# Optimization experiments

Hardware: AMD Instinct MI355X
Metric: run time of the kernel (lower is better)

## Reference

```python
import jax, jax.numpy as jnp
import numpy as np

N_NODES = 50000
N_EDGES = 400000
D_IN = 128
D_H = 128
N_CLASSES = 20
N_GRAPHS = 256
EPS_BN = 1e-5


def _lin_params(key, d_in, d_out, scale=0.05):
    kw, kb = jax.random.split(key)
    W = jax.random.normal(kw, (d_in, d_out), jnp.float32) * scale
    b = jax.random.normal(kb, (d_out,), jnp.float32) * scale
    return W, b


def setup_inputs() -> dict:
    key = jax.random.key(0)
    ks = jax.random.split(key, 20)
    inp = {
        "x": jax.random.normal(ks[0], (N_NODES, D_IN), jnp.float32),
        "edge_index": jax.random.randint(ks[1], (2, N_EDGES), 0, N_NODES, jnp.int32),
        "batch": jnp.sort(jax.random.randint(ks[2], (N_NODES,), 0, N_GRAPHS, jnp.int32)),
    }
    kidx = 3
    for li, d_in in zip((1, 2, 3), (D_IN, D_H, D_H)):
        for nm in ("q", "k", "v", "s"):
            W, b = _lin_params(ks[kidx], d_in, D_H)
            kidx += 1
            inp[f"W{nm}{li}"] = W
            inp[f"b{nm}{li}"] = b
        inp[f"gamma{li}"] = jnp.ones((D_H,), jnp.float32)
        inp[f"beta{li}"] = jnp.zeros((D_H,), jnp.float32)
    Wl, bl = _lin_params(ks[kidx], D_H, N_CLASSES)
    inp["Wlin"] = Wl
    inp["blin"] = bl
    return inp


def _segment_softmax(logits, seg, n):
    m = jax.ops.segment_max(logits, seg, num_segments=n)
    e = jnp.exp(logits - m[seg])
    s = jax.ops.segment_sum(e, seg, num_segments=n)
    return e / (s[seg] + 1e-16)


def _transformer_conv(x, src, dst, Wq, bq, Wk, bk, Wv, bv, Ws, bs):
    # heads=1, concat=True, root_weight=True (PyG TransformerConv defaults)
    q = x @ Wq + bq  # [N, d]
    k = x @ Wk + bk
    v = x @ Wv + bv
    d = q.shape[-1]
    logits = jnp.sum(q[dst] * k[src], axis=-1) / jnp.sqrt(jnp.float32(d))  # [E]
    alpha = _segment_softmax(logits, dst, x.shape[0])
    out = jax.ops.segment_sum(alpha[:, None] * v[src], dst, num_segments=x.shape[0])
    return out + x @ Ws + bs


def _batch_norm(x, gamma, beta):
    mu = jnp.mean(x, axis=0)
    var = jnp.var(x, axis=0)
    return gamma * (x - mu) * jax.lax.rsqrt(var + EPS_BN) + beta


def _global_mean_pool(x, batch, n_graphs):
    sums = jax.ops.segment_sum(x, batch, num_segments=n_graphs)
    cnt = jax.ops.segment_sum(jnp.ones((x.shape[0],), x.dtype), batch, num_segments=n_graphs)
    return sums / jnp.maximum(cnt, 1.0)[:, None]


def reference(x, edge_index, batch,
              Wq1, bq1, Wk1, bk1, Wv1, bv1, Ws1, bs1, gamma1, beta1,
              Wq2, bq2, Wk2, bk2, Wv2, bv2, Ws2, bs2, gamma2, beta2,
              Wq3, bq3, Wk3, bk3, Wv3, bv3, Ws3, bs3, gamma3, beta3,
              Wlin, blin):
    src, dst = edge_index[0], edge_index[1]
    h = _transformer_conv(x, src, dst, Wq1, bq1, Wk1, bk1, Wv1, bv1, Ws1, bs1)
    h = jax.nn.relu(_batch_norm(h, gamma1, beta1))  # dropout inactive (eval)
    h = _transformer_conv(h, src, dst, Wq2, bq2, Wk2, bk2, Wv2, bv2, Ws2, bs2)
    h = jax.nn.relu(_batch_norm(h, gamma2, beta2))
    h = _transformer_conv(h, src, dst, Wq3, bq3, Wk3, bk3, Wv3, bv3, Ws3, bs3)
    h = jax.nn.relu(_batch_norm(h, gamma3, beta3))
    g = _global_mean_pool(h, batch, N_GRAPHS)  # [G, d]
    return g @ Wlin + blin  # [G, num_classes]
```

## Files before the change

### kernel.cpp

```cpp
#include <hip/hip_runtime.h>

#define N_NODES 50000
#define N_EDGES 400000
#define DH 128
#define N_GRAPHS 256

#define SCAN_CHUNK 512
#define N_CHUNKS ((N_NODES + SCAN_CHUNK - 1) / SCAN_CHUNK)
#define ATTN_BLOCKS ((N_NODES + 15) / 16)
#define POOL_CHUNKS ((N_NODES + 63) / 64)

typedef __bf16 bf16x8 __attribute__((ext_vector_type(8)));
typedef float f32x4 __attribute__((ext_vector_type(4)));
typedef _Float16 f16x2 __attribute__((ext_vector_type(2)));
typedef _Float16 f16x8 __attribute__((ext_vector_type(8)));

#define DEV __device__ __forceinline__

#if defined(__has_builtin)
#if __has_builtin(__builtin_amdgcn_fdot2)
#define HAS_FDOT2 1
#endif
#endif

DEV float fdot2acc(f16x2 a, f16x2 b, float c) {
#ifdef HAS_FDOT2
  return __builtin_amdgcn_fdot2(a, b, c, false);
#else
  return (float)a.x * (float)b.x + (float)a.y * (float)b.y + c;
#endif
}

DEV unsigned short f2bf(float f) {
  union { float f; unsigned int i; } v; v.f = f;
  unsigned int x = v.i;
  unsigned int r = (x + 0x7fffu + ((x >> 16) & 1u)) >> 16;
  return (unsigned short)r;
}

struct WPtrs { const float* w[12]; };

__global__ void repack_kernel(WPtrs wp, unsigned short* __restrict__ WB,
                              int* __restrict__ deg, int* __restrict__ counter, int N) {
  int mat = blockIdx.y;
  int m = blockIdx.x * 256 + threadIdx.x;
  int j = m & 7;
  int lane = (m >> 3) & 63;
  int ct = (m >> 9) & 7;
  int kk = m >> 12;
  int i = kk * 32 + (lane >> 4) * 8 + j;
  int o = ct * 16 + (lane & 15);
  WB[mat * 16384 + m] = f2bf(wp.w[mat][i * 128 + o]);
  if (mat == 0) {
    for (int idx = m; idx < N; idx += 16384) deg[idx] = 0;
    if (m == 0) *counter = 0;
  }
}

__global__ void deg_count(const int* __restrict__ ei, int* __restrict__ deg, int E) {
  int e = blockIdx.x * 256 + threadIdx.x;
  if (e < E) atomicAdd(&deg[ei[E + e]], 1);
}

__global__ __launch_bounds__(256) void scan_sum(const int* __restrict__ deg,
                                                int* __restrict__ partials, int N) {
  __shared__ int red[256];
  int b = blockIdx.x, t = threadIdx.x;
  int base = b * SCAN_CHUNK + t * 2;
  int s = 0;
  if (base + 1 < N) { int2 v = *reinterpret_cast<const int2*>(deg + base); s = v.x + v.y; }
  else if (base < N) s = deg[base];
  red[t] = s;
  __syncthreads();
  for (int off = 128; off; off >>= 1) {
    if (t < off) red[t] += red[t + off];
    __syncthreads();
  }
  if (t == 0) partials[b] = red[0];
}

__global__ __launch_bounds__(128) void scan_partials(int* __restrict__ partials) {
  __shared__ int s[128];
  int t = threadIdx.x;
  int v = (t < N_CHUNKS) ? partials[t] : 0;
  s[t] = v;
  __syncthreads();
  for (int off = 1; off < 128; off <<= 1) {
    int o = (t >= off) ? s[t - off] : 0;
    __syncthreads();
    s[t] += o;
    __syncthreads();
  }
  if (t < N_CHUNKS) partials[t] = s[t] - v;
}

__global__ __launch_bounds__(256) void scan_apply(const int* __restrict__ deg,
                                                  const int* __restrict__ partials,
                                                  int* __restrict__ rowptr,
                                                  int* __restrict__ cursor, int N, int E) {
  __shared__ int s[256];
  int b = blockIdx.x, t = threadIdx.x;
  int base = b * SCAN_CHUNK + t * 2;
  int d0 = 0, d1 = 0;
  if (base + 1 < N) { int2 v = *reinterpret_cast<const int2*>(deg + base); d0 = v.x; d1 = v.y; }
  else if (base < N) d0 = deg[base];
  int local = d0 + d1;
  s[t] = local;
  __syncthreads();
  for (int off = 1; off < 256; off <<= 1) {
    int o = (t >= off) ? s[t - off] : 0;
    __syncthreads();
    s[t] += o;
    __syncthreads();
  }
  int offp = partials[b] + s[t] - local;
  if (base < N)     { rowptr[base] = offp;          cursor[base] = offp; }
  if (base + 1 < N) { rowptr[base + 1] = offp + d0; cursor[base + 1] = offp + d0; }
  if (b == 0 && t == 0) rowptr[N] = E;
}

__global__ void csr_scatter(const int* __restrict__ ei, int* __restrict__ cursor,
                            int* __restrict__ adj, int E) {
  int e = blockIdx.x * 256 + threadIdx.x;
  if (e < E) {
    int dst = ei[E + e];
    int pos = atomicAdd(&cursor[dst], 1);
    adj[pos] = ei[e];
  }
}

struct GemmOut { _Float16* Y[4]; const float* bias[4]; };

#define LDP 136

__global__ __launch_bounds__(256) void gemm_proj(
    const float* __restrict__ Xf,
    const _Float16* __restrict__ Hin,
    const float* __restrict__ scale, const float* __restrict__ shift,
    const unsigned short* __restrict__ WB4,
    GemmOut go, int useBN, int N)
{
  __shared__ __align__(16) unsigned short xs[64 * LDP];

  const int t = threadIdx.x;
  const int rowBase = blockIdx.x * 64;
  const int igc = (t & 15) * 8;

  if (useBN) {
    float4 sc0 = *reinterpret_cast<const float4*>(scale + igc);
    float4 sc1 = *reinterpret_cast<const float4*>(scale + igc + 4);
    float4 sh0 = *reinterpret_cast<const float4*>(shift + igc);
    float4 sh1 = *reinterpret_cast<const float4*>(shift + igc + 4);
#pragma unroll
    for (int j = 0; j < 4; ++j) {
      int v = t + 256 * j;
      int r = v >> 4;
      int grow = rowBase + r;
      ushort4 o0 = make_ushort4(0, 0, 0, 0), o1 = make_ushort4(0, 0, 0, 0);
      if (grow < N) {
        f16x8 hv = *reinterpret_cast<const f16x8*>(Hin + (size_t)grow * 128 + igc);
        o0.x = f2bf(fmaxf((float)hv[0] * sc0.x + sh0.x, 0.f));
        o0.y = f2bf(fmaxf((float)hv[1] * sc0.y + sh0.y, 0.f));
        o0.z = f2bf(fmaxf((float)hv[2] * sc0.z + sh0.z, 0.f));
        o0.w = f2bf(fmaxf((float)hv[3] * sc0.w + sh0.w, 0.f));
        o1.x = f2bf(fmaxf((float)hv[4] * sc1.x + sh1.x, 0.f));
        o1.y = f2bf(fmaxf((float)hv[5] * sc1.y + sh1.y, 0.f));
        o1.z = f2bf(fmaxf((float)hv[6] * sc1.z + sh1.z, 0.f));
        o1.w = f2bf(fmaxf((float)hv[7] * sc1.w + sh1.w, 0.f));
      }
      *reinterpret_cast<ushort4*>(&xs[r * LDP + igc]) = o0;
      *reinterpret_cast<ushort4*>(&xs[r * LDP + igc + 4]) = o1;
    }
  } else {
#pragma unroll
    for (int j = 0; j < 4; ++j) {
      int v = t + 256 * j;
      int r = v >> 4;
      int grow = rowBase + r;
      ushort4 o0 = make_ushort4(0, 0, 0, 0), o1 = make_ushort4(0, 0, 0, 0);
      if (grow < N) {
        float4 a = *reinterpret_cast<const float4*>(Xf + (size_t)grow * 128 + igc);
        float4 b = *reinterpret_cast<const float4*>(Xf + (size_t)grow * 128 + igc + 4);
        o0.x = f2bf(a.x); o0.y = f2bf(a.y); o0.z = f2bf(a.z); o0.w = f2bf(a.w);
        o1.x = f2bf(b.x); o1.y = f2bf(b.y); o1.z = f2bf(b.z); o1.w = f2bf(b.w);
      }
      *reinterpret_cast<ushort4*>(&xs[r * LDP + igc]) = o0;
      *reinterpret_cast<ushort4*>(&xs[r * LDP + igc + 4]) = o1;
    }
  }
  __syncthreads();

  const int wave = t >> 6;
  const int lane = t & 63;
  const int ln16 = lane & 15;
  const int quad = lane >> 4;
  const int r0 = wave * 16;

  bf16x8 afrag[4];
#pragma unroll
  for (int kk = 0; kk < 4; ++kk)
    afrag[kk] = *reinterpret_cast<const bf16x8*>(&xs[(r0 + ln16) * LDP + kk * 32 + quad * 8]);

  for (int proj = 0; proj < 4; ++proj) {
    const unsigned short* __restrict__ WB = WB4 + proj * 16384;
    const float* __restrict__ bias = go.bias[proj];

    f32x4 acc[8] = {};
#pragma unroll
    for (int kk = 0; kk < 4; ++kk) {
#pragma unroll
      for (int ct = 0; ct < 8; ++ct) {
        bf16x8 b = *reinterpret_cast<const bf16x8*>(WB + ((kk * 8 + ct) * 64 + lane) * 8);
        acc[ct] = __builtin_amdgcn_mfma_f32_16x16x32_bf16(afrag[kk], b, acc[ct], 0, 0, 0);
      }
    }

    _Float16* __restrict__ Yh = go.Y[proj];
#pragma unroll
    for (int ct = 0; ct < 8; ++ct) {
      int col = ct * 16 + ln16;
      float bv = bias[col];
#pragma unroll
      for (int reg = 0; reg < 4; ++reg) {
        int grow = rowBase + r0 + quad * 4 + reg;
        if (grow < N) Yh[(size_t)grow * 128 + col] = (_Float16)(acc[ct][reg] + bv);
      }
    }
  }
}

__global__ __launch_bounds__(256) void node_attn(
    const int* __restrict__ rowptr, const int* __restrict__ adj,
    const _Float16* __restrict__ Q, const _Float16* __restrict__ K,
    const _Float16* __restrict__ V, _Float16* __restrict__ H,
    float* __restrict__ Pbuf, int N)
{
  __shared__ float lsum[16][128];
  __shared__ float lsq[16][128];
  int t = threadIdx.x;
  int w = t >> 4, lane = t & 15;
  int n = blockIdx.x * 16 + w;
  bool valid = n < N;
  int nn = valid ? n : 0;
  int p0 = 0, p1 = 0;
  if (valid) { p0 = rowptr[n]; p1 = rowptr[n + 1]; }

  f16x8 qv = *reinterpret_cast<const f16x8*>(Q + (size_t)nn * 128 + lane * 8);
  f16x2 q0 = {qv[0], qv[1]}, q1 = {qv[2], qv[3]}, q2 = {qv[4], qv[5]}, q3 = {qv[6], qv[7]};

  float m = -INFINITY, s = 0.f;
  float acc[8] = {};

  int p = p0;
  for (; p + 1 < p1; p += 2) {
    int s0 = adj[p], s1 = adj[p + 1];
    f16x8 k0 = *reinterpret_cast<const f16x8*>(K + (size_t)s0 * 128 + lane * 8);
    f16x8 k1 = *reinterpret_cast<const f16x8*>(K + (size_t)s1 * 128 + lane * 8);
    float d0 = fdot2acc(q0, (f16x2){k0[0], k0[1]},
               fdot2acc(q1, (f16x2){k0[2], k0[3]},
               fdot2acc(q2, (f16x2){k0[4], k0[5]},
               fdot2acc(q3, (f16x2){k0[6], k0[7]}, 0.f))));
    float d1 = fdot2acc(q0, (f16x2){k1[0], k1[1]},
               fdot2acc(q1, (f16x2){k1[2], k1[3]},
               fdot2acc(q2, (f16x2){k1[4], k1[5]},
               fdot2acc(q3, (f16x2){k1[6], k1[7]}, 0.f))));
#pragma unroll
    for (int off = 8; off; off >>= 1) {
      d0 += __shfl_xor(d0, off, 16);
      d1 += __shfl_xor(d1, off, 16);
    }
    float l0 = d0 * 0.08838834764831845f;
    float l1 = d1 * 0.08838834764831845f;
    float mn = fmaxf(m, fmaxf(l0, l1));
    float sc = __expf(m - mn);
    float w0 = __expf(l0 - mn);
    float w1 = __expf(l1 - mn);
    f16x8 v0 = *reinterpret_cast<const f16x8*>(V + (size_t)s0 * 128 + lane * 8);
    f16x8 v1 = *reinterpret_cast<const f16x8*>(V + (size_t)s1 * 128 + lane * 8);
#pragma unroll
    for (int i = 0; i < 8; ++i)
      acc[i] = acc[i] * sc + w0 * (float)v0[i] + w1 * (float)v1[i];
    s = s * sc + w0 + w1;
    m = mn;
  }
  if (p < p1) {
    int s0 = adj[p];
    f16x8 k0 = *reinterpret_cast<const f16x8*>(K + (size_t)s0 * 128 + lane * 8);
    float d0 = fdot2acc(q0, (f16x2){k0[0], k0[1]},
               fdot2acc(q1, (f16x2){k0[2], k0[3]},
               fdot2acc(q2, (f16x2){k0[4], k0[5]},
               fdot2acc(q3, (f16x2){k0[6], k0[7]}, 0.f))));
#pragma unroll
    for (int off = 8; off; off >>= 1) d0 += __shfl_xor(d0, off, 16);
    float l0 = d0 * 0.08838834764831845f;
    float mn = fmaxf(m, l0);
    float sc = __expf(m - mn);
    float w0 = __expf(l0 - mn);
    f16x8 v0 = *reinterpret_cast<const f16x8*>(V + (size_t)s0 * 128 + lane * 8);
#pragma unroll
    for (int i = 0; i < 8; ++i)
      acc[i] = acc[i] * sc + w0 * (float)v0[i];
    s = s * sc + w0;
    m = mn;
  }

  float h[8];
#pragma unroll
  for (int i = 0; i < 8; ++i) h[i] = 0.f;
  if (valid) {
    float inv = 1.0f / (s + 1e-16f);
    f16x8 hh = *reinterpret_cast<const f16x8*>(H + (size_t)n * 128 + lane * 8);
    f16x8 ho;
#pragma unroll
    for (int i = 0; i < 8; ++i) {
      h[i] = (float)hh[i] + acc[i] * inv;
      ho[i] = (_Float16)h[i];
    }
    *reinterpret_cast<f16x8*>(H + (size_t)n * 128 + lane * 8) = ho;
  }

#pragma unroll
  for (int i = 0; i < 8; i += 4) {
    float4 hv = make_float4(h[i], h[i + 1], h[i + 2], h[i + 3]);
    float4 h2 = make_float4(hv.x * hv.x, hv.y * hv.y, hv.z * hv.z, hv.w * hv.w);
    *reinterpret_cast<float4*>(&lsum[w][lane * 8 + i]) = hv;
    *reinterpret_cast<float4*>(&lsq[w][lane * 8 + i]) = h2;
  }
  __syncthreads();

  int f = t & 127;
  float a = 0.f;
  if (t < 128) {
#pragma unroll
    for (int n16 = 0; n16 < 16; ++n16) a += lsum[n16][f];
  } else {
#pragma unroll
    for (int n16 = 0; n16 < 16; ++n16) a += lsq[n16][f];
  }
  Pbuf[(size_t)blockIdx.x * 256 + t] = a;
}

__global__ __launch_bounds__(256) void bn_reduce(
    const float* __restrict__ Pbuf, float* __restrict__ partial,
    int* __restrict__ counter,
    const float* __restrict__ gamma, const float* __restrict__ beta,
    float* __restrict__ scale, float* __restrict__ shift, int N)
{
  int t = threadIdx.x;
  float s0 = 0.f, s1 = 0.f, s2 = 0.f, s3 = 0.f;
  int r = blockIdx.x;
  for (; r + 192 < ATTN_BLOCKS; r += 256) {
    s0 += Pbuf[(size_t)(r      ) * 256 + t];
    s1 += Pbuf[(size_t)(r +  64) * 256 + t];
    s2 += Pbuf[(size_t)(r + 128) * 256 + t];
    s3 += Pbuf[(size_t)(r + 192) * 256 + t];
  }
  for (; r < ATTN_BLOCKS; r += 64) s0 += Pbuf[(size_t)r * 256 + t];
  partial[blockIdx.x * 256 + t] = s0 + s1 + s2 + s3;

  __threadfence();
  __shared__ int isLast;
  if (t == 0) isLast = (atomicAdd(counter, 1) == 63);
  __syncthreads();
  if (!isLast) return;
  __threadfence();

  __shared__ float red[256];
  float a0 = 0.f, a1 = 0.f, a2 = 0.f, a3 = 0.f;
#pragma unroll
  for (int b = 0; b < 64; b += 4) {
    a0 += partial[(b + 0) * 256 + t];
    a1 += partial[(b + 1) * 256 + t];
    a2 += partial[(b + 2) * 256 + t];
    a3 += partial[(b + 3) * 256 + t];
  }
  red[t] = a0 + a1 + a2 + a3;
  __syncthreads();
  if (t == 0) *counter = 0;
  if (t < 128) {
    float mean = red[t] / (float)N;
    float var = red[t + 128] / (float)N - mean * mean;
    var = fmaxf(var, 0.f);
    float sc = gamma[t] * rsqrtf(var + 1e-5f);
    scale[t] = sc;
    shift[t] = beta[t] - mean * sc;
  }
}

__global__ __launch_bounds__(256) void pool_chunk(
    const _Float16* __restrict__ H, const float* __restrict__ scale,
    const float* __restrict__ shift, const int* __restrict__ batch,
    float* __restrict__ pooled, int N)
{
  int f = threadIdx.x & 127, half = threadIdx.x >> 7;
  int base = blockIdx.x * 64;
  int lim = min(base + 64, N);
  float sc = scale[f], sh = shift[f];
  int curg = -1; float s = 0.f;
  for (int row = base + half; row < lim; row += 2) {
    int g = batch[row];
    if (g != curg) {
      if (curg >= 0) unsafeAtomicAdd(pooled + curg * 128 + f, s);
      curg = g; s = 0.f;
    }
    s += fmaxf((float)H[(size_t)row * 128 + f] * sc + sh, 0.f);
  }
  if (curg >= 0) unsafeAtomicAdd(pooled + curg * 128 + f, s);
}

__global__ __launch_bounds__(64) void final_linear(
    const float* __restrict__ pooled, const int* __restrict__ batch,
    const float* __restrict__ Wlin, const float* __restrict__ blin,
    float* __restrict__ out, int N)
{
  int g = blockIdx.x;
  int c = threadIdx.x;
  int lo = 0, hi = N;
  while (lo < hi) { int mid = (lo + hi) >> 1; if (batch[mid] < g) lo = mid + 1; else hi = mid; }
  int start = lo;
  hi = N;
  while (lo < hi) { int mid = (lo + hi) >> 1; if (batch[mid] < g + 1) lo = mid + 1; else hi = mid; }
  float inv = 1.0f / fmaxf((float)(lo - start), 1.f);
  if (c < 20) {
    float acc = 0.f;
#pragma unroll 4
    for (int i = 0; i < 128; ++i)
      acc += pooled[g * 128 + i] * Wlin[i * 20 + c];
    out[g * 20 + c] = acc * inv + blin[c];
  }
}

extern "C" void kernel_launch(void* const* d_in, const int* in_sizes, int n_in,
                              void* d_out, int out_size, void* d_ws, size_t ws_size,
                              hipStream_t stream)
{
  const int N = N_NODES, E = N_EDGES, G = N_GRAPHS;

  const float* x = (const float*)d_in[0];
  const int* ei = (const int*)d_in[1];
  const int* batch = (const int*)d_in[2];
  const float* Wlin = (const float*)d_in[33];
  const float* blin = (const float*)d_in[34];

  char* ws = (char*)d_ws;
  size_t off = 0;
  auto alloc = [&](size_t bytes) -> void* {
    void* p = ws + off;
    off = (off + bytes + 255) & ~(size_t)255;
    return p;
  };
  unsigned short* WB = (unsigned short*)alloc(12 * 16384 * sizeof(unsigned short));
  _Float16* Qh  = (_Float16*)alloc((size_t)N * 128 * 2);
  _Float16* Kh  = (_Float16*)alloc((size_t)N * 128 * 2);
  _Float16* Vh  = (_Float16*)alloc((size_t)N * 128 * 2);
  _Float16* Hh  = (_Float16*)alloc((size_t)N * 128 * 2);
  int* deg      = (int*)alloc((size_t)N * 4);
  int* rowptr   = (int*)alloc((size_t)(N + 1) * 4);
  int* cursor   = (int*)alloc((size_t)N * 4);
  int* adj      = (int*)alloc((size_t)E * 4);
  int* partials = (int*)alloc((size_t)N_CHUNKS * 4);
  int* counter  = (int*)alloc(256);
  float* Pbuf   = (float*)alloc((size_t)ATTN_BLOCKS * 256 * 4);
  float* bnpart = (float*)alloc((size_t)64 * 256 * 4);
  float* scale  = (float*)alloc(128 * 4);
  float* shift  = (float*)alloc(128 * 4);
  float* pooled = (float*)alloc((size_t)G * 128 * 4);

  WPtrs wp;
  for (int L = 0; L < 3; ++L) {
    wp.w[L * 4 + 0] = (const float*)d_in[3 + L * 10 + 0];
    wp.w[L * 4 + 1] = (const float*)d_in[3 + L * 10 + 2];
    wp.w[L * 4 + 2] = (const float*)d_in[3 + L * 10 + 4];
    wp.w[L * 4 + 3] = (const float*)d_in[3 + L * 10 + 6];
  }
  repack_kernel<<<dim3(64, 12), 256, 0, stream>>>(wp, WB, deg, counter, N);

  deg_count<<<(E + 255) / 256, 256, 0, stream>>>(ei, deg, E);
  scan_sum<<<N_CHUNKS, 256, 0, stream>>>(deg, partials, N);
  scan_partials<<<1, 128, 0, stream>>>(partials);
  scan_apply<<<N_CHUNKS, 256, 0, stream>>>(deg, partials, rowptr, cursor, N, E);
  csr_scatter<<<(E + 255) / 256, 256, 0, stream>>>(ei, cursor, adj, E);
  hipMemsetAsync(pooled, 0, (size_t)G * 128 * 4, stream);

  for (int L = 0; L < 3; ++L) {
    GemmOut go;
    go.Y[0] = Qh; go.Y[1] = Kh; go.Y[2] = Vh; go.Y[3] = Hh;
    go.bias[0] = (const float*)d_in[3 + L * 10 + 1];
    go.bias[1] = (const float*)d_in[3 + L * 10 + 3];
    go.bias[2] = (const float*)d_in[3 + L * 10 + 5];
    go.bias[3] = (const float*)d_in[3 + L * 10 + 7];
    gemm_proj<<<(N + 63) / 64, 256, 0, stream>>>(
        x, Hh, scale, shift, WB + L * 4 * 16384, go, (L > 0) ? 1 : 0, N);

    node_attn<<<ATTN_BLOCKS, 256, 0, stream>>>(rowptr, adj, Qh, Kh, Vh, Hh, Pbuf, N);

    bn_reduce<<<64, 256, 0, stream>>>(Pbuf, bnpart, counter,
        (const float*)d_in[3 + L * 10 + 8],
        (const float*)d_in[3 + L * 10 + 9],
        scale, shift, N);

    if (L == 2) {
      pool_chunk<<<POOL_CHUNKS, 256, 0, stream>>>(Hh, scale, shift, batch, pooled, N);
      final_linear<<<G, 64, 0, stream>>>(pooled, batch, Wlin, blin, (float*)d_out, N);
    }
  }
}
```

Before: 453.8 us.

## Split projection GEMM across grid y, prepack bf16 input, widen BN reduce

Moves the fp32/BN-ReLU to bf16 conversion into a separate elementwise kernel that writes a bf16 activation buffer. The projection GEMM is then launched with one block per (row tile, projection) so the four Q/K/V/skip projections run in parallel blocks, giving more blocks. The BN partial reduction grows from 64 to 256 blocks. This adds an extra pass that writes and re-reads the activations, plus an extra launch, and each of the four projection blocks reloads the same input tile. In place, the gemm_proj launches go from 782 blocks to 3128.

```diff
diff --git a/kernel.cpp b/kernel.cpp
--- a/kernel.cpp
+++ b/kernel.cpp
@@ -9,6 +9,7 @@
 #define N_CHUNKS ((N_NODES + SCAN_CHUNK - 1) / SCAN_CHUNK)
 #define ATTN_BLOCKS ((N_NODES + 15) / 16)
 #define POOL_CHUNKS ((N_NODES + 63) / 64)
+#define XB_BLOCKS ((N_NODES * 128 / 8 + 255) / 256)
 
 typedef __bf16 bf16x8 __attribute__((ext_vector_type(8)));
 typedef float f32x4 __attribute__((ext_vector_type(4)));
@@ -57,6 +58,42 @@
   }
 }
 
+__global__ __launch_bounds__(256) void xb_from_x(const float* __restrict__ x,
+                                                 unsigned short* __restrict__ Xb) {
+  int i8 = (blockIdx.x * 256 + threadIdx.x) * 8;
+  float4 a = *reinterpret_cast<const float4*>(x + i8);
+  float4 b = *reinterpret_cast<const float4*>(x + i8 + 4);
+  ushort4 o0, o1;
+  o0.x = f2bf(a.x); o0.y = f2bf(a.y); o0.z = f2bf(a.z); o0.w = f2bf(a.w);
+  o1.x = f2bf(b.x); o1.y = f2bf(b.y); o1.z = f2bf(b.z); o1.w = f2bf(b.w);
+  *reinterpret_cast<ushort4*>(Xb + i8) = o0;
+  *reinterpret_cast<ushort4*>(Xb + i8 + 4) = o1;
+}
+
+__global__ __launch_bounds__(256) void xb_from_h(const _Float16* __restrict__ H,
+                                                 const float* __restrict__ scale,
+                                                 const float* __restrict__ shift,
+                                                 unsigned short* __restrict__ Xb) {
+  int i8 = (blockIdx.x * 256 + threadIdx.x) * 8;
+  int f = i8 & 127;
+  f16x8 hv = *reinterpret_cast<const f16x8*>(H + i8);
+  float4 sc0 = *reinterpret_cast<const float4*>(scale + f);
+  float4 sc1 = *reinterpret_cast<const float4*>(scale + f + 4);
+  float4 sh0 = *reinterpret_cast<const float4*>(shift + f);
+  float4 sh1 = *reinterpret_cast<const float4*>(shift + f + 4);
+  ushort4 o0, o1;
+  o0.x = f2bf(fmaxf((float)hv[0] * sc0.x + sh0.x, 0.f));
+  o0.y = f2bf(fmaxf((float)hv[1] * sc0.y + sh0.y, 0.f));
+  o0.z = f2bf(fmaxf((float)hv[2] * sc0.z + sh0.z, 0.f));
+  o0.w = f2bf(fmaxf((float)hv[3] * sc0.w + sh0.w, 0.f));
+  o1.x = f2bf(fmaxf((float)hv[4] * sc1.x + sh1.x, 0.f));
+  o1.y = f2bf(fmaxf((float)hv[5] * sc1.y + sh1.y, 0.f));
+  o1.z = f2bf(fmaxf((float)hv[6] * sc1.z + sh1.z, 0.f));
+  o1.w = f2bf(fmaxf((float)hv[7] * sc1.w + sh1.w, 0.f));
+  *reinterpret_cast<ushort4*>(Xb + i8) = o0;
+  *reinterpret_cast<ushort4*>(Xb + i8 + 4) = o1;
+}
+
 __global__ void deg_count(const int* __restrict__ ei, int* __restrict__ deg, int E) {
   int e = blockIdx.x * 256 + threadIdx.x;
   if (e < E) atomicAdd(&deg[ei[E + e]], 1);
@@ -134,59 +171,25 @@
 #define LDP 136
 
 __global__ __launch_bounds__(256) void gemm_proj(
-    const float* __restrict__ Xf,
-    const _Float16* __restrict__ Hin,
-    const float* __restrict__ scale, const float* __restrict__ shift,
+    const unsigned short* __restrict__ Xb,
     const unsigned short* __restrict__ WB4,
-    GemmOut go, int useBN, int N)
+    GemmOut go, int N)
 {
   __shared__ __align__(16) unsigned short xs[64 * LDP];
 
   const int t = threadIdx.x;
   const int rowBase = blockIdx.x * 64;
   const int igc = (t & 15) * 8;
-
-  if (useBN) {
-    float4 sc0 = *reinterpret_cast<const float4*>(scale + igc);
-    float4 sc1 = *reinterpret_cast<const float4*>(scale + igc + 4);
-    float4 sh0 = *reinterpret_cast<const float4*>(shift + igc);
-    float4 sh1 = *reinterpret_cast<const float4*>(shift + igc + 4);
-#pragma unroll
-    for (int j = 0; j < 4; ++j) {
-      int v = t + 256 * j;
-      int r = v >> 4;
-      int grow = rowBase + r;
-      ushort4 o0 = make_ushort4(0, 0, 0, 0), o1 = make_ushort4(0, 0, 0, 0);
-      if (grow < N) {
-        f16x8 hv = *reinterpret_cast<const f16x8*>(Hin + (size_t)grow * 128 + igc);
-        o0.x = f2bf(fmaxf((float)hv[0] * sc0.x + sh0.x, 0.f));
-        o0.y = f2bf(fmaxf((float)hv[1] * sc0.y + sh0.y, 0.f));
-        o0.z = f2bf(fmaxf((float)hv[2] * sc0.z + sh0.z, 0.f));
-        o0.w = f2bf(fmaxf((float)hv[3] * sc0.w + sh0.w, 0.f));
-        o1.x = f2bf(fmaxf((float)hv[4] * sc1.x + sh1.x, 0.f));
-        o1.y = f2bf(fmaxf((float)hv[5] * sc1.y + sh1.y, 0.f));
-        o1.z = f2bf(fmaxf((float)hv[6] * sc1.z + sh1.z, 0.f));
-        o1.w = f2bf(fmaxf((float)hv[7] * sc1.w + sh1.w, 0.f));
-      }
-      *reinterpret_cast<ushort4*>(&xs[r * LDP + igc]) = o0;
-      *reinterpret_cast<ushort4*>(&xs[r * LDP + igc + 4]) = o1;
-    }
-  } else {
-#pragma unroll
-    for (int j = 0; j < 4; ++j) {
-      int v = t + 256 * j;
-      int r = v >> 4;
-      int grow = rowBase + r;
-      ushort4 o0 = make_ushort4(0, 0, 0, 0), o1 = make_ushort4(0, 0, 0, 0);
-      if (grow < N) {
-        float4 a = *reinterpret_cast<const float4*>(Xf + (size_t)grow * 128 + igc);
-        float4 b = *reinterpret_cast<const float4*>(Xf + (size_t)grow * 128 + igc + 4);
-        o0.x = f2bf(a.x); o0.y = f2bf(a.y); o0.z = f2bf(a.z); o0.w = f2bf(a.w);
-        o1.x = f2bf(b.x); o1.y = f2bf(b.y); o1.z = f2bf(b.z); o1.w = f2bf(b.w);
-      }
-      *reinterpret_cast<ushort4*>(&xs[r * LDP + igc]) = o0;
-      *reinterpret_cast<ushort4*>(&xs[r * LDP + igc + 4]) = o1;
-    }
+  const int proj = blockIdx.y;
+
+#pragma unroll
+  for (int j = 0; j < 4; ++j) {
+    int v = t + 256 * j;
+    int r = v >> 4;
+    int grow = rowBase + r;
+    uint4 val = make_uint4(0u, 0u, 0u, 0u);
+    if (grow < N) val = *reinterpret_cast<const uint4*>(Xb + (size_t)grow * 128 + igc);
+    *reinterpret_cast<uint4*>(&xs[r * LDP + igc]) = val;
   }
   __syncthreads();
 
@@ -196,35 +199,29 @@
   const int quad = lane >> 4;
   const int r0 = wave * 16;
 
-  bf16x8 afrag[4];
-#pragma unroll
-  for (int kk = 0; kk < 4; ++kk)
-    afrag[kk] = *reinterpret_cast<const bf16x8*>(&xs[(r0 + ln16) * LDP + kk * 32 + quad * 8]);
-
-  for (int proj = 0; proj < 4; ++proj) {
-    const unsigned short* __restrict__ WB = WB4 + proj * 16384;
-    const float* __restrict__ bias = go.bias[proj];
-
-    f32x4 acc[8] = {};
-#pragma unroll
-    for (int kk = 0; kk < 4; ++kk) {
-#pragma unroll
-      for (int ct = 0; ct < 8; ++ct) {
-        bf16x8 b = *reinterpret_cast<const bf16x8*>(WB + ((kk * 8 + ct) * 64 + lane) * 8);
-        acc[ct] = __builtin_amdgcn_mfma_f32_16x16x32_bf16(afrag[kk], b, acc[ct], 0, 0, 0);
-      }
+  const unsigned short* __restrict__ WB = WB4 + proj * 16384;
+  const float* __restrict__ bias = go.bias[proj];
+
+  f32x4 acc[8] = {};
+#pragma unroll
+  for (int kk = 0; kk < 4; ++kk) {
+    bf16x8 a = *reinterpret_cast<const bf16x8*>(&xs[(r0 + ln16) * LDP + kk * 32 + quad * 8]);
+#pragma unroll
+    for (int ct = 0; ct < 8; ++ct) {
+      bf16x8 b = *reinterpret_cast<const bf16x8*>(WB + ((kk * 8 + ct) * 64 + lane) * 8);
+      acc[ct] = __builtin_amdgcn_mfma_f32_16x16x32_bf16(a, b, acc[ct], 0, 0, 0);
     }
-
-    _Float16* __restrict__ Yh = go.Y[proj];
-#pragma unroll
-    for (int ct = 0; ct < 8; ++ct) {
-      int col = ct * 16 + ln16;
-      float bv = bias[col];
-#pragma unroll
-      for (int reg = 0; reg < 4; ++reg) {
-        int grow = rowBase + r0 + quad * 4 + reg;
-        if (grow < N) Yh[(size_t)grow * 128 + col] = (_Float16)(acc[ct][reg] + bv);
-      }
+  }
+
+  _Float16* __restrict__ Yh = go.Y[proj];
+#pragma unroll
+  for (int ct = 0; ct < 8; ++ct) {
+    int col = ct * 16 + ln16;
+    float bv = bias[col];
+#pragma unroll
+    for (int reg = 0; reg < 4; ++reg) {
+      int grow = rowBase + r0 + quad * 4 + reg;
+      if (grow < N) Yh[(size_t)grow * 128 + col] = (_Float16)(acc[ct][reg] + bv);
     }
   }
 }
@@ -347,28 +344,22 @@
     float* __restrict__ scale, float* __restrict__ shift, int N)
 {
   int t = threadIdx.x;
-  float s0 = 0.f, s1 = 0.f, s2 = 0.f, s3 = 0.f;
-  int r = blockIdx.x;
-  for (; r + 192 < ATTN_BLOCKS; r += 256) {
-    s0 += Pbuf[(size_t)(r      ) * 256 + t];
-    s1 += Pbuf[(size_t)(r +  64) * 256 + t];
-    s2 += Pbuf[(size_t)(r + 128) * 256 + t];
-    s3 += Pbuf[(size_t)(r + 192) * 256 + t];
-  }
-  for (; r < ATTN_BLOCKS; r += 64) s0 += Pbuf[(size_t)r * 256 + t];
-  partial[blockIdx.x * 256 + t] = s0 + s1 + s2 + s3;
+  float s = 0.f;
+  for (int r = blockIdx.x; r < ATTN_BLOCKS; r += 256)
+    s += Pbuf[(size_t)r * 256 + t];
+  partial[blockIdx.x * 256 + t] = s;
 
   __threadfence();
   __shared__ int isLast;
-  if (t == 0) isLast = (atomicAdd(counter, 1) == 63);
+  if (t == 0) isLast = (atomicAdd(counter, 1) == 255);
   __syncthreads();
   if (!isLast) return;
   __threadfence();
 
   __shared__ float red[256];
   float a0 = 0.f, a1 = 0.f, a2 = 0.f, a3 = 0.f;
-#pragma unroll
-  for (int b = 0; b < 64; b += 4) {
+#pragma unroll 4
+  for (int b = 0; b < 256; b += 4) {
     a0 += partial[(b + 0) * 256 + t];
     a1 += partial[(b + 1) * 256 + t];
     a2 += partial[(b + 2) * 256 + t];
@@ -450,6 +441,7 @@
     return p;
   };
   unsigned short* WB = (unsigned short*)alloc(12 * 16384 * sizeof(unsigned short));
+  unsigned short* Xb = (unsigned short*)alloc((size_t)N * 128 * 2);
   _Float16* Qh  = (_Float16*)alloc((size_t)N * 128 * 2);
   _Float16* Kh  = (_Float16*)alloc((size_t)N * 128 * 2);
   _Float16* Vh  = (_Float16*)alloc((size_t)N * 128 * 2);
@@ -461,7 +453,7 @@
   int* partials = (int*)alloc((size_t)N_CHUNKS * 4);
   int* counter  = (int*)alloc(256);
   float* Pbuf   = (float*)alloc((size_t)ATTN_BLOCKS * 256 * 4);
-  float* bnpart = (float*)alloc((size_t)64 * 256 * 4);
+  float* bnpart = (float*)alloc((size_t)256 * 256 * 4);
   float* scale  = (float*)alloc(128 * 4);
   float* shift  = (float*)alloc(128 * 4);
   float* pooled = (float*)alloc((size_t)G * 128 * 4);
@@ -483,18 +475,20 @@
   hipMemsetAsync(pooled, 0, (size_t)G * 128 * 4, stream);
 
   for (int L = 0; L < 3; ++L) {
+    if (L == 0) xb_from_x<<<XB_BLOCKS, 256, 0, stream>>>(x, Xb);
+    else        xb_from_h<<<XB_BLOCKS, 256, 0, stream>>>(Hh, scale, shift, Xb);
+
     GemmOut go;
     go.Y[0] = Qh; go.Y[1] = Kh; go.Y[2] = Vh; go.Y[3] = Hh;
     go.bias[0] = (const float*)d_in[3 + L * 10 + 1];
     go.bias[1] = (const float*)d_in[3 + L * 10 + 3];
     go.bias[2] = (const float*)d_in[3 + L * 10 + 5];
     go.bias[3] = (const float*)d_in[3 + L * 10 + 7];
-    gemm_proj<<<(N + 63) / 64, 256, 0, stream>>>(
-        x, Hh, scale, shift, WB + L * 4 * 16384, go, (L > 0) ? 1 : 0, N);
+    gemm_proj<<<dim3((N + 63) / 64, 4), 256, 0, stream>>>(Xb, WB + L * 4 * 16384, go, N);
 
     node_attn<<<ATTN_BLOCKS, 256, 0, stream>>>(rowptr, adj, Qh, Kh, Vh, Hh, Pbuf, N);
 
-    bn_reduce<<<64, 256, 0, stream>>>(Pbuf, bnpart, counter,
+    bn_reduce<<<256, 256, 0, stream>>>(Pbuf, bnpart, counter,
         (const float*)d_in[3 + L * 10 + 8],
         (const float*)d_in[3 + L * 10 + 9],
         scale, shift, N);
```

New measurement: 531.7 us. 17.2% more time.
